# Optimization experiments

Hardware: AMD Instinct MI355X
Metric: run time of the kernel (lower is better)

## Reference

```python
import jax, jax.numpy as jnp
import numpy as np

G = 8          # n_games
D_IN = 512     # per-game input dim (equal for all games)
H1 = 1024
H2 = 1024
A = 128        # max_actions
B = 8192       # batch rows


def setup_inputs() -> dict:
    key = jax.random.key(0)
    ks = jax.random.split(key, 9)
    state = jax.random.normal(ks[0], (B, D_IN), dtype=jnp.float32)
    idx = jax.random.randint(ks[1], (B,), 0, G, dtype=jnp.int32)
    # per-game input linears: uniform(-1/sqrt(fan_in), 1/sqrt(fan_in))
    lim1 = 1.0 / np.sqrt(D_IN)
    W1 = jax.random.uniform(ks[2], (G, D_IN, H1), minval=-lim1, maxval=lim1, dtype=jnp.float32)
    b1 = jax.random.uniform(ks[3], (G, H1), minval=-lim1, maxval=lim1, dtype=jnp.float32)
    # shared linear
    lim2 = 1.0 / np.sqrt(H1)
    W2 = jax.random.uniform(ks[4], (H1, H2), minval=-lim2, maxval=lim2, dtype=jnp.float32)
    b2 = jax.random.uniform(ks[5], (H2,), minval=-lim2, maxval=lim2, dtype=jnp.float32)
    # per-game output heads: uniform(-0.003, 0.003)
    W3 = jax.random.uniform(ks[6], (G, H2, A), minval=-0.003, maxval=0.003, dtype=jnp.float32)
    b3 = jax.random.uniform(ks[7], (G, A), minval=-0.003, maxval=0.003, dtype=jnp.float32)
    return {"state": state, "idx": idx, "W1": W1, "b1": b1, "W2": W2, "b2": b2, "W3": W3, "b3": b3}


def reference(state, idx, W1, b1, W2, b2, W3, b3):
    # Torch code concatenates per-game groups in sorted-unique-idx order,
    # i.e. a stable permutation of rows by idx; reproduce exactly.
    perm = jnp.argsort(idx, stable=True)          # [B]
    s = state[perm]                               # [B, D_IN]
    g = idx[perm]                                 # [B] game of each permuted row
    # routed first layer: compute all games then gather per-row game
    h1_all = jnp.einsum('bd,gdh->bgh', s, W1) + b1            # [B, G, H1]
    h1 = jax.nn.relu(jnp.take_along_axis(h1_all, g[:, None, None], axis=1)[:, 0, :])  # [B, H1]
    h_f = jax.nn.relu(h1 @ W2 + b2)                            # [B, H2]
    a = jnp.tanh(jnp.einsum('bh,gha->bga', h_f, W3) + b3)      # [B, G, A]
    # NOTE: original gathers heads with the ORIGINAL (unpermuted) idx,
    # even though rows of `a` are in permuted order. Reproduce faithfully.
    out = jnp.take_along_axis(a, idx[:, None, None], axis=1)[:, 0, :]  # [B, A]
    return out
```

## Files before the change

### kernel.cpp

```cpp
#include <hip/hip_runtime.h>
#include <math.h>

#define G_GAMES 8
#define D_IN 512
#define H1 1024
#define H2 1024
#define A_DIM 128
#define B_ROWS 8192

typedef short bf16x8 __attribute__((ext_vector_type(8)));
typedef float f32x4 __attribute__((ext_vector_type(4)));

#define WS_OFF   0u
#define WS_PERM  256u
#define WS_SPERM 33280u
#define WS_W1T   (WS_SPERM + B_ROWS*D_IN*2u)
#define WS_W2T   (WS_W1T + G_GAMES*D_IN*H1*2u)
#define WS_W3T   (WS_W2T + (unsigned)H1*H2*2u)
#define WS_H1    (WS_W3T + G_GAMES*H2*A_DIM*2u)
#define WS_HF    WS_SPERM

__device__ __forceinline__ unsigned short f2bf(float x) {
  union { float f; unsigned int u; } v; v.f = x;
  unsigned int r = v.u + 0x7fffu + ((v.u >> 16) & 1u);
  return (unsigned short)(r >> 16);
}

__device__ __forceinline__ void async_load16(const void* gptr, void* ldsptr) {
  __builtin_amdgcn_global_load_lds(
      (const __attribute__((address_space(1))) unsigned int*)gptr,
      (__attribute__((address_space(3))) unsigned int*)ldsptr,
      16, 0, 0);
}

__device__ void sort_256(const int* __restrict__ idx, int* __restrict__ perm,
                         int* __restrict__ off) {
  __shared__ int wtot[4][9];
  __shared__ int wbase[4][9];
  __shared__ int offs[9];
  const int t = threadIdx.x, lane = t & 63, wave = t >> 6;
  int my[32];
#pragma unroll
  for (int i = 0; i < 8; ++i) {
    const int4 a = *(const int4*)(idx + t * 32 + i * 4);
    my[i*4+0] = a.x; my[i*4+1] = a.y; my[i*4+2] = a.z; my[i*4+3] = a.w;
  }
  int local[8] = {0,0,0,0,0,0,0,0};
#pragma unroll
  for (int i = 0; i < 32; ++i) local[my[i]]++;
  int incl[8];
#pragma unroll
  for (int g = 0; g < 8; ++g) {
    int v = local[g];
#pragma unroll
    for (int d = 1; d < 64; d <<= 1) {
      const int n = __shfl_up(v, d);
      if (lane >= d) v += n;
    }
    incl[g] = v;
  }
  if (lane == 63) {
#pragma unroll
    for (int g = 0; g < 8; ++g) wtot[wave][g] = incl[g];
  }
  __syncthreads();
  if (t < 8) {
    int s = 0;
#pragma unroll
    for (int w = 0; w < 4; ++w) { wbase[w][t] = s; s += wtot[w][t]; }
    wtot[0][t] = s;
  }
  __syncthreads();
  if (t == 0) {
    int s = 0;
#pragma unroll
    for (int g = 0; g < 8; ++g) { offs[g] = s; off[g] = s; s += wtot[0][g]; }
    offs[8] = s; off[8] = s;
  }
  __syncthreads();
  int start[8];
#pragma unroll
  for (int g = 0; g < 8; ++g)
    start[g] = offs[g] + wbase[wave][g] + (incl[g] - local[g]);
#pragma unroll
  for (int i = 0; i < 32; ++i) {
    const int g = my[i];
    perm[start[g]++] = t * 32 + i;
  }
}

__device__ void trans_tile(const float* __restrict__ in,
                           unsigned short* __restrict__ out,
                           int R, int C, int xt, int yt, int z) {
  in  += (size_t)z * R * C;
  out += (size_t)z * R * C;
  __shared__ float tile[64][65];
  const int c0 = xt * 64, r0 = yt * 64;
  const int tx = threadIdx.x & 63, ty = threadIdx.x >> 6;
#pragma unroll
  for (int rr = ty; rr < 64; rr += 4)
    tile[rr][tx] = in[(size_t)(r0 + rr) * C + c0 + tx];
  __syncthreads();
#pragma unroll
  for (int cc = ty; cc < 64; cc += 4)
    out[(size_t)(c0 + cc) * R + r0 + tx] = f2bf(tile[tx][cc]);
}

__global__ __launch_bounds__(256) void k_pre1(const float* __restrict__ W1,
                                              const float* __restrict__ W2,
                                              const float* __restrict__ W3,
                                              const int* __restrict__ idx,
                                              unsigned short* __restrict__ W1T,
                                              unsigned short* __restrict__ W2T,
                                              unsigned short* __restrict__ W3T,
                                              int* __restrict__ perm,
                                              int* __restrict__ off) {
  const int b = blockIdx.x;
  if (b < 1024) {
    const int z = b >> 7, r = b & 127;
    trans_tile(W1, W1T, D_IN, H1, r & 15, r >> 4, z);
  } else if (b < 1280) {
    const int r = b - 1024;
    trans_tile(W2, W2T, H1, H2, r & 15, r >> 4, 0);
  } else if (b < 1536) {
    const int r = (b - 1280) & 31, z = (b - 1280) >> 5;
    trans_tile(W3, W3T, H2, A_DIM, r & 1, r >> 1, z);
  } else {
    sort_256(idx, perm, off);
  }
}

__global__ __launch_bounds__(256) void k_gather(const float* __restrict__ state,
                                                const int* __restrict__ perm,
                                                unsigned short* __restrict__ sPerm) {
  const int p = blockIdx.x * 2 + (threadIdx.x >> 7);
  const int c = (threadIdx.x & 127) << 2;
  const int src = perm[p];
  const float4 v = *(const float4*)(state + (size_t)src * D_IN + c);
  ushort4 o;
  o.x = f2bf(v.x); o.y = f2bf(v.y); o.z = f2bf(v.z); o.w = f2bf(v.w);
  *(ushort4*)(sPerm + (size_t)p * D_IN + c) = o;
}

__device__ __forceinline__ void gemm_core128(const unsigned short* const* aP,
                                             const unsigned short* const* bP,
                                             char* A, char* Bc,
                                             int KTOT, int tid, f32x4 acc[4][4]) {
  const int lane = tid & 63, wave = tid >> 6;
  const int wm = wave & 1, wn = wave >> 1;
  const int mA = wm * 64 + (lane & 15);
  const int nB = wn * 64 + (lane & 15);
  const int quad = lane >> 4;
  const int sw = lane & 15;
  for (int k0 = 0; k0 < KTOT; k0 += 128) {
    __syncthreads();
#pragma unroll
    for (int c = 0; c < 8; ++c) {
      const int rbase = wave * 32 + c * 4;
      async_load16(aP[c] + k0, A + rbase * 256);
      async_load16(bP[c] + k0, Bc + rbase * 256);
    }
    __syncthreads();
#pragma unroll
    for (int ks = 0; ks < 4; ++ks) {
      const int u = (((ks * 4 + quad) ^ sw) << 4);
      bf16x8 aF[4], bF[4];
#pragma unroll
      for (int i = 0; i < 4; ++i) {
        aF[i] = *(const bf16x8*)(A + (mA + i * 16) * 256 + u);
        bF[i] = *(const bf16x8*)(Bc + (nB + i * 16) * 256 + u);
      }
#pragma unroll
      for (int i = 0; i < 4; ++i)
#pragma unroll
        for (int j = 0; j < 4; ++j)
          acc[i][j] = __builtin_amdgcn_mfma_f32_16x16x32_bf16(aF[i], bF[j], acc[i][j], 0, 0, 0);
    }
  }
}

__device__ __forceinline__ bool seg_map(const int* __restrict__ off, int T,
                                        int& g, int& seg1, int& row0) {
  int base = 0;
  for (int gg = 0; gg < 8; ++gg) {
    const int s = off[gg], e = off[gg + 1];
    const int nt = (e - s + 127) >> 7;
    if (T < base + nt) { g = gg; seg1 = e; row0 = s + (T - base) * 128; return true; }
    base += nt;
  }
  return false;
}

__device__ __forceinline__ bool seg_map32(const int* __restrict__ off, int T,
                                          int& g, int& seg1, int& row0) {
  int base = 0;
  for (int gg = 0; gg < 8; ++gg) {
    const int s = off[gg], e = off[gg + 1];
    const int nt = (e - s + 31) >> 5;
    if (T < base + nt) { g = gg; seg1 = e; row0 = s + (T - base) * 32; return true; }
    base += nt;
  }
  return false;
}

__global__ __launch_bounds__(256) void k_gemm1(const unsigned short* __restrict__ sPerm,
                                               const unsigned short* __restrict__ W1T,
                                               const float* __restrict__ b1,
                                               const int* __restrict__ off,
                                               unsigned short* __restrict__ h1out) {
  __shared__ unsigned short ldsA[128 * 128];
  __shared__ unsigned short ldsB[128 * 128];
  int g, seg1, row0;
  if (!seg_map(off, blockIdx.x, g, seg1, row0)) return;
  const int col0 = blockIdx.y * 128;
  const int tid = threadIdx.x, lane = tid & 63, wave = tid >> 6;
  const int quad = lane >> 4, sw = lane & 15;
  const unsigned short* aP[8];
  const unsigned short* bP[8];
#pragma unroll
  for (int c = 0; c < 8; ++c) {
    const int rl = wave * 32 + c * 4 + quad;
    const int srcoff = ((sw ^ (rl & 15)) << 3);
    int p = row0 + rl;
    if (p > seg1 - 1) p = seg1 - 1;
    aP[c] = sPerm + (size_t)p * D_IN + srcoff;
    bP[c] = W1T + (size_t)g * H1 * D_IN + (size_t)(col0 + rl) * D_IN + srcoff;
  }
  f32x4 acc[4][4] = {};
  gemm_core128(aP, bP, (char*)ldsA, (char*)ldsB, D_IN, tid, acc);
  const int wm = wave & 1, wn = wave >> 1;
  const float* bg = b1 + g * H1;
#pragma unroll
  for (int j = 0; j < 4; ++j) {
    const int n = col0 + wn * 64 + j * 16 + sw;
    const float bj = bg[n];
#pragma unroll
    for (int i = 0; i < 4; ++i) {
      const int rbase = row0 + wm * 64 + i * 16 + (quad << 2);
#pragma unroll
      for (int r = 0; r < 4; ++r) {
        const int p = rbase + r;
        if (p < seg1) {
          float v = acc[i][j][r] + bj;
          v = fmaxf(v, 0.0f);
          h1out[(size_t)p * H1 + n] = f2bf(v);
        }
      }
    }
  }
}

__global__ __launch_bounds__(256) void k_gemm2(const unsigned short* __restrict__ h1in,
                                               const unsigned short* __restrict__ W2T,
                                               const float* __restrict__ b2,
                                               unsigned short* __restrict__ hfout) {
  __shared__ unsigned short ldsA[128 * 128];
  __shared__ unsigned short ldsB[128 * 128];
  const int row0 = blockIdx.x * 128, col0 = blockIdx.y * 128;
  const int tid = threadIdx.x, lane = tid & 63, wave = tid >> 6;
  const int quad = lane >> 4, sw = lane & 15;
  const unsigned short* aP[8];
  const unsigned short* bP[8];
#pragma unroll
  for (int c = 0; c < 8; ++c) {
    const int rl = wave * 32 + c * 4 + quad;
    const int srcoff = ((sw ^ (rl & 15)) << 3);
    aP[c] = h1in + (size_t)(row0 + rl) * H1 + srcoff;
    bP[c] = W2T + (size_t)(col0 + rl) * H1 + srcoff;
  }
  f32x4 acc[4][4] = {};
  gemm_core128(aP, bP, (char*)ldsA, (char*)ldsB, H1, tid, acc);
  const int wm = wave & 1, wn = wave >> 1;
#pragma unroll
  for (int j = 0; j < 4; ++j) {
    const int n = col0 + wn * 64 + j * 16 + sw;
    const float bj = b2[n];
#pragma unroll
    for (int i = 0; i < 4; ++i) {
      const int rbase = row0 + wm * 64 + i * 16 + (quad << 2);
#pragma unroll
      for (int r = 0; r < 4; ++r) {
        float v = acc[i][j][r] + bj;
        v = fmaxf(v, 0.0f);
        hfout[(size_t)(rbase + r) * H2 + n] = f2bf(v);
      }
    }
  }
}

__global__ __launch_bounds__(256) void k_gemm3(const unsigned short* __restrict__ hf,
                                               const unsigned short* __restrict__ W3T,
                                               const float* __restrict__ b3,
                                               const int* __restrict__ off,
                                               const int* __restrict__ perm,
                                               float* __restrict__ outp) {
  __shared__ unsigned short ldsA[32 * 128];
  __shared__ unsigned short ldsB[128 * 128];
  int g, seg1, row0;
  if (!seg_map32(off, blockIdx.x, g, seg1, row0)) return;
  const int tid = threadIdx.x, lane = tid & 63, wave = tid >> 6;
  const int wm = wave & 1, wn = wave >> 1;
  const int quad = lane >> 4, sw = lane & 15;
  const unsigned short* aP[2];
  const unsigned short* bP[8];
#pragma unroll
  for (int c = 0; c < 2; ++c) {
    const int rl = wave * 8 + c * 4 + quad;
    const int srcoff = ((sw ^ (rl & 15)) << 3);
    int q = row0 + rl;
    if (q > seg1 - 1) q = seg1 - 1;
    aP[c] = hf + (size_t)perm[q] * H2 + srcoff;
  }
#pragma unroll
  for (int c = 0; c < 8; ++c) {
    const int rl = wave * 32 + c * 4 + quad;
    const int srcoff = ((sw ^ (rl & 15)) << 3);
    bP[c] = W3T + (size_t)g * A_DIM * H2 + (size_t)rl * H2 + srcoff;
  }
  char* A = (char*)ldsA;
  char* Bc = (char*)ldsB;
  const int mA = wm * 16 + sw;
  const int nB = wn * 64 + sw;
  f32x4 acc[4] = {};
  for (int k0 = 0; k0 < H2; k0 += 128) {
    __syncthreads();
#pragma unroll
    for (int c = 0; c < 2; ++c)
      async_load16(aP[c] + k0, A + (wave * 8 + c * 4) * 256);
#pragma unroll
    for (int c = 0; c < 8; ++c)
      async_load16(bP[c] + k0, Bc + (wave * 32 + c * 4) * 256);
    __syncthreads();
#pragma unroll
    for (int ks = 0; ks < 4; ++ks) {
      const int u = (((ks * 4 + quad) ^ sw) << 4);
      const bf16x8 aF = *(const bf16x8*)(A + mA * 256 + u);
      bf16x8 bF[4];
#pragma unroll
      for (int j = 0; j < 4; ++j)
        bF[j] = *(const bf16x8*)(Bc + (nB + j * 16) * 256 + u);
#pragma unroll
      for (int j = 0; j < 4; ++j)
        acc[j] = __builtin_amdgcn_mfma_f32_16x16x32_bf16(aF, bF[j], acc[j], 0, 0, 0);
    }
  }
  const float* bg = b3 + g * A_DIM;
#pragma unroll
  for (int j = 0; j < 4; ++j) {
    const int n = wn * 64 + j * 16 + sw;
    const float bj = bg[n];
    const int qbase = row0 + wm * 16 + (quad << 2);
#pragma unroll
    for (int r = 0; r < 4; ++r) {
      const int q2 = qbase + r;
      if (q2 < seg1)
        outp[(size_t)perm[q2] * A_DIM + n] = tanhf(acc[j][r] + bj);
    }
  }
}

extern "C" void kernel_launch(void* const* d_in, const int* in_sizes, int n_in,
                              void* d_out, int out_size, void* d_ws, size_t ws_size,
                              hipStream_t stream) {
  (void)in_sizes; (void)n_in; (void)out_size; (void)ws_size;
  const float* state = (const float*)d_in[0];
  const int*   idx   = (const int*)d_in[1];
  const float* W1    = (const float*)d_in[2];
  const float* b1    = (const float*)d_in[3];
  const float* W2    = (const float*)d_in[4];
  const float* b2    = (const float*)d_in[5];
  const float* W3    = (const float*)d_in[6];
  const float* b3    = (const float*)d_in[7];
  float* outp = (float*)d_out;
  char* ws = (char*)d_ws;
  int* off  = (int*)(ws + WS_OFF);
  int* perm = (int*)(ws + WS_PERM);
  unsigned short* sPerm = (unsigned short*)(ws + WS_SPERM);
  unsigned short* W1T   = (unsigned short*)(ws + WS_W1T);
  unsigned short* W2T   = (unsigned short*)(ws + WS_W2T);
  unsigned short* W3T   = (unsigned short*)(ws + WS_W3T);
  unsigned short* h1    = (unsigned short*)(ws + WS_H1);
  unsigned short* hf    = (unsigned short*)(ws + WS_HF);

  hipLaunchKernelGGL(k_pre1, dim3(1537), dim3(256), 0, stream,
                     W1, W2, W3, idx, W1T, W2T, W3T, perm, off);
  hipLaunchKernelGGL(k_gather, dim3(B_ROWS / 2), dim3(256), 0, stream, state, perm, sPerm);
  hipLaunchKernelGGL(k_gemm1, dim3(72, 8), dim3(256), 0, stream, sPerm, W1T, b1, off, h1);
  hipLaunchKernelGGL(k_gemm2, dim3(64, 8), dim3(256), 0, stream, h1, W2T, b2, hf);
  hipLaunchKernelGGL(k_gemm3, dim3(264), dim3(256), 0, stream, hf, W3T, b3, off, perm, outp);
}
```

Before: 172.3 us.

## Double-buffer GEMM K-loop with BK=64 and stage epilogues through LDS

Replaces the single-buffered BK=128 load-sync-compute loop in all three GEMMs with a double-buffered BK=64 pipeline, so async global-to-LDS loads of the next K slice are issued while MFMAs run on the current one, with one barrier per iteration. The swizzle changes to an 8-chunk XOR pattern to suit 128-byte LDS rows. The epilogues now stage bias+ReLU/tanh results in LDS and write 16-byte coalesced rows instead of scattered 2- or 4-byte stores. This costs extra LDS traffic and barriers in the epilogue, and smaller K slices mean more loop iterations.

```diff
diff --git a/kernel.cpp b/kernel.cpp
--- a/kernel.cpp
+++ b/kernel.cpp
@@ -142,33 +142,46 @@
   *(ushort4*)(sPerm + (size_t)p * D_IN + c) = o;
 }
 
-__device__ __forceinline__ void gemm_core128(const unsigned short* const* aP,
+template <int KTOT>
+__device__ __forceinline__ void gemm_db_core(const unsigned short* const* aP,
                                              const unsigned short* const* bP,
-                                             char* A, char* Bc,
-                                             int KTOT, int tid, f32x4 acc[4][4]) {
+                                             char* smem, int tid, f32x4 acc[4][4]) {
   const int lane = tid & 63, wave = tid >> 6;
   const int wm = wave & 1, wn = wave >> 1;
-  const int mA = wm * 64 + (lane & 15);
-  const int nB = wn * 64 + (lane & 15);
-  const int quad = lane >> 4;
-  const int sw = lane & 15;
-  for (int k0 = 0; k0 < KTOT; k0 += 128) {
+  const int sw = lane & 15, quad = lane >> 4;
+  const int mA = wm * 64 + sw;
+  const int nB = wn * 64 + sw;
+  char* A0 = smem;          char* A1 = smem + 16384;
+  char* B0 = smem + 32768;  char* B1 = smem + 49152;
+  const int NIT = KTOT >> 6;
+#pragma unroll
+  for (int c = 0; c < 4; ++c) {
+    async_load16(aP[c], A0 + (wave * 32 + c * 8) * 128);
+    async_load16(bP[c], B0 + (wave * 32 + c * 8) * 128);
+  }
+#pragma unroll 2
+  for (int k = 0; k < NIT; ++k) {
     __syncthreads();
-#pragma unroll
-    for (int c = 0; c < 8; ++c) {
-      const int rbase = wave * 32 + c * 4;
-      async_load16(aP[c] + k0, A + rbase * 256);
-      async_load16(bP[c] + k0, Bc + rbase * 256);
-    }
-    __syncthreads();
-#pragma unroll
-    for (int ks = 0; ks < 4; ++ks) {
-      const int u = (((ks * 4 + quad) ^ sw) << 4);
+    char* A = (k & 1) ? A1 : A0;
+    char* B = (k & 1) ? B1 : B0;
+    if (k + 1 < NIT) {
+      char* An = (k & 1) ? A0 : A1;
+      char* Bn = (k & 1) ? B0 : B1;
+      const int koff = (k + 1) << 6;
+#pragma unroll
+      for (int c = 0; c < 4; ++c) {
+        async_load16(aP[c] + koff, An + (wave * 32 + c * 8) * 128);
+        async_load16(bP[c] + koff, Bn + (wave * 32 + c * 8) * 128);
+      }
+    }
+#pragma unroll
+    for (int ks = 0; ks < 2; ++ks) {
+      const int u = ((((ks << 2) + quad) ^ (sw & 7)) << 4);
       bf16x8 aF[4], bF[4];
 #pragma unroll
       for (int i = 0; i < 4; ++i) {
-        aF[i] = *(const bf16x8*)(A + (mA + i * 16) * 256 + u);
-        bF[i] = *(const bf16x8*)(Bc + (nB + i * 16) * 256 + u);
+        aF[i] = *(const bf16x8*)(A + (mA + i * 16) * 128 + u);
+        bF[i] = *(const bf16x8*)(B + (nB + i * 16) * 128 + u);
       }
 #pragma unroll
       for (int i = 0; i < 4; ++i)
@@ -203,89 +216,95 @@
   return false;
 }
 
+__device__ __forceinline__ void epilogue_bf16(char* smem, const f32x4 acc[4][4],
+                                              const float* bj, int tid,
+                                              unsigned short* __restrict__ outp,
+                                              size_t ldOut, int row0, int col0,
+                                              int vrows) {
+  const int lane = tid & 63, wave = tid >> 6;
+  const int wm = wave & 1, wn = wave >> 1;
+  const int sw = lane & 15, quad = lane >> 4;
+  __syncthreads();
+#pragma unroll
+  for (int i = 0; i < 4; ++i)
+#pragma unroll
+    for (int j = 0; j < 4; ++j)
+#pragma unroll
+      for (int r = 0; r < 4; ++r) {
+        const int row = wm * 64 + i * 16 + quad * 4 + r;
+        const int col = wn * 64 + j * 16 + sw;
+        const float v = fmaxf(acc[i][j][r] + bj[j], 0.0f);
+        *(unsigned short*)(smem + row * 264 + col * 2) = f2bf(v);
+      }
+  __syncthreads();
+#pragma unroll
+  for (int q = 0; q < 8; ++q) {
+    const int idxq = q * 256 + tid;
+    const int row = idxq >> 4, ch = idxq & 15;
+    if (row < vrows) {
+      const uint2 lo = *(const uint2*)(smem + row * 264 + ch * 16);
+      const uint2 hi = *(const uint2*)(smem + row * 264 + ch * 16 + 8);
+      uint4 v; v.x = lo.x; v.y = lo.y; v.z = hi.x; v.w = hi.y;
+      *(uint4*)((char*)outp + ((size_t)(row0 + row) * ldOut + col0 + ch * 8) * 2) = v;
+    }
+  }
+}
+
 __global__ __launch_bounds__(256) void k_gemm1(const unsigned short* __restrict__ sPerm,
                                                const unsigned short* __restrict__ W1T,
                                                const float* __restrict__ b1,
                                                const int* __restrict__ off,
                                                unsigned short* __restrict__ h1out) {
-  __shared__ unsigned short ldsA[128 * 128];
-  __shared__ unsigned short ldsB[128 * 128];
+  __shared__ char smem[65536];
   int g, seg1, row0;
   if (!seg_map(off, blockIdx.x, g, seg1, row0)) return;
   const int col0 = blockIdx.y * 128;
   const int tid = threadIdx.x, lane = tid & 63, wave = tid >> 6;
-  const int quad = lane >> 4, sw = lane & 15;
-  const unsigned short* aP[8];
-  const unsigned short* bP[8];
-#pragma unroll
-  for (int c = 0; c < 8; ++c) {
-    const int rl = wave * 32 + c * 4 + quad;
-    const int srcoff = ((sw ^ (rl & 15)) << 3);
+  const int gcol = ((lane & 7) ^ (lane >> 3)) << 3;
+  const unsigned short* aP[4];
+  const unsigned short* bP[4];
+#pragma unroll
+  for (int c = 0; c < 4; ++c) {
+    const int rl = wave * 32 + c * 8 + (lane >> 3);
     int p = row0 + rl;
     if (p > seg1 - 1) p = seg1 - 1;
-    aP[c] = sPerm + (size_t)p * D_IN + srcoff;
-    bP[c] = W1T + (size_t)g * H1 * D_IN + (size_t)(col0 + rl) * D_IN + srcoff;
+    aP[c] = sPerm + (size_t)p * D_IN + gcol;
+    bP[c] = W1T + (size_t)g * H1 * D_IN + (size_t)(col0 + rl) * D_IN + gcol;
   }
   f32x4 acc[4][4] = {};
-  gemm_core128(aP, bP, (char*)ldsA, (char*)ldsB, D_IN, tid, acc);
-  const int wm = wave & 1, wn = wave >> 1;
+  gemm_db_core<D_IN>(aP, bP, smem, tid, acc);
+  const int wn = wave >> 1, sw = lane & 15;
   const float* bg = b1 + g * H1;
-#pragma unroll
-  for (int j = 0; j < 4; ++j) {
-    const int n = col0 + wn * 64 + j * 16 + sw;
-    const float bj = bg[n];
-#pragma unroll
-    for (int i = 0; i < 4; ++i) {
-      const int rbase = row0 + wm * 64 + i * 16 + (quad << 2);
-#pragma unroll
-      for (int r = 0; r < 4; ++r) {
-        const int p = rbase + r;
-        if (p < seg1) {
-          float v = acc[i][j][r] + bj;
-          v = fmaxf(v, 0.0f);
-          h1out[(size_t)p * H1 + n] = f2bf(v);
-        }
-      }
-    }
-  }
+  float bj[4];
+#pragma unroll
+  for (int j = 0; j < 4; ++j) bj[j] = bg[col0 + wn * 64 + j * 16 + sw];
+  const int vrows = min(128, seg1 - row0);
+  epilogue_bf16(smem, acc, bj, tid, h1out, H1, row0, col0, vrows);
 }
 
 __global__ __launch_bounds__(256) void k_gemm2(const unsigned short* __restrict__ h1in,
                                                const unsigned short* __restrict__ W2T,
                                                const float* __restrict__ b2,
                                                unsigned short* __restrict__ hfout) {
-  __shared__ unsigned short ldsA[128 * 128];
-  __shared__ unsigned short ldsB[128 * 128];
+  __shared__ char smem[65536];
   const int row0 = blockIdx.x * 128, col0 = blockIdx.y * 128;
   const int tid = threadIdx.x, lane = tid & 63, wave = tid >> 6;
-  const int quad = lane >> 4, sw = lane & 15;
-  const unsigned short* aP[8];
-  const unsigned short* bP[8];
-#pragma unroll
-  for (int c = 0; c < 8; ++c) {
-    const int rl = wave * 32 + c * 4 + quad;
-    const int srcoff = ((sw ^ (rl & 15)) << 3);
-    aP[c] = h1in + (size_t)(row0 + rl) * H1 + srcoff;
-    bP[c] = W2T + (size_t)(col0 + rl) * H1 + srcoff;
+  const int gcol = ((lane & 7) ^ (lane >> 3)) << 3;
+  const unsigned short* aP[4];
+  const unsigned short* bP[4];
+#pragma unroll
+  for (int c = 0; c < 4; ++c) {
+    const int rl = wave * 32 + c * 8 + (lane >> 3);
+    aP[c] = h1in + (size_t)(row0 + rl) * H1 + gcol;
+    bP[c] = W2T + (size_t)(col0 + rl) * H1 + gcol;
   }
   f32x4 acc[4][4] = {};
-  gemm_core128(aP, bP, (char*)ldsA, (char*)ldsB, H1, tid, acc);
-  const int wm = wave & 1, wn = wave >> 1;
-#pragma unroll
-  for (int j = 0; j < 4; ++j) {
-    const int n = col0 + wn * 64 + j * 16 + sw;
-    const float bj = b2[n];
-#pragma unroll
-    for (int i = 0; i < 4; ++i) {
-      const int rbase = row0 + wm * 64 + i * 16 + (quad << 2);
-#pragma unroll
-      for (int r = 0; r < 4; ++r) {
-        float v = acc[i][j][r] + bj;
-        v = fmaxf(v, 0.0f);
-        hfout[(size_t)(rbase + r) * H2 + n] = f2bf(v);
-      }
-    }
-  }
+  gemm_db_core<H1>(aP, bP, smem, tid, acc);
+  const int wn = wave >> 1, sw = lane & 15;
+  float bj[4];
+#pragma unroll
+  for (int j = 0; j < 4; ++j) bj[j] = b2[col0 + wn * 64 + j * 16 + sw];
+  epilogue_bf16(smem, acc, bj, tid, hfout, H2, row0, col0, 128);
 }
 
 __global__ __launch_bounds__(256) void k_gemm3(const unsigned short* __restrict__ hf,
@@ -294,67 +313,79 @@
                                                const int* __restrict__ off,
                                                const int* __restrict__ perm,
                                                float* __restrict__ outp) {
-  __shared__ unsigned short ldsA[32 * 128];
-  __shared__ unsigned short ldsB[128 * 128];
+  __shared__ char smem[40960];
   int g, seg1, row0;
   if (!seg_map32(off, blockIdx.x, g, seg1, row0)) return;
   const int tid = threadIdx.x, lane = tid & 63, wave = tid >> 6;
   const int wm = wave & 1, wn = wave >> 1;
-  const int quad = lane >> 4, sw = lane & 15;
-  const unsigned short* aP[2];
-  const unsigned short* bP[8];
-#pragma unroll
-  for (int c = 0; c < 2; ++c) {
-    const int rl = wave * 8 + c * 4 + quad;
-    const int srcoff = ((sw ^ (rl & 15)) << 3);
-    int q = row0 + rl;
-    if (q > seg1 - 1) q = seg1 - 1;
-    aP[c] = hf + (size_t)perm[q] * H2 + srcoff;
-  }
-#pragma unroll
-  for (int c = 0; c < 8; ++c) {
-    const int rl = wave * 32 + c * 4 + quad;
-    const int srcoff = ((sw ^ (rl & 15)) << 3);
-    bP[c] = W3T + (size_t)g * A_DIM * H2 + (size_t)rl * H2 + srcoff;
-  }
-  char* A = (char*)ldsA;
-  char* Bc = (char*)ldsB;
+  const int sw = lane & 15, quad = lane >> 4;
+  const int gcol = ((lane & 7) ^ (lane >> 3)) << 3;
+  int q0 = row0 + wave * 8 + (lane >> 3);
+  if (q0 > seg1 - 1) q0 = seg1 - 1;
+  const unsigned short* aP = hf + (size_t)perm[q0] * H2 + gcol;
+  const unsigned short* bP[4];
+#pragma unroll
+  for (int c = 0; c < 4; ++c) {
+    const int rl = wave * 32 + c * 8 + (lane >> 3);
+    bP[c] = W3T + (size_t)g * A_DIM * H2 + (size_t)rl * H2 + gcol;
+  }
+  char* A0 = smem;         char* A1 = smem + 4096;
+  char* B0 = smem + 8192;  char* B1 = smem + 24576;
   const int mA = wm * 16 + sw;
   const int nB = wn * 64 + sw;
   f32x4 acc[4] = {};
-  for (int k0 = 0; k0 < H2; k0 += 128) {
+  async_load16(aP, A0 + (wave * 8) * 128);
+#pragma unroll
+  for (int c = 0; c < 4; ++c)
+    async_load16(bP[c], B0 + (wave * 32 + c * 8) * 128);
+#pragma unroll 2
+  for (int k = 0; k < (H2 >> 6); ++k) {
     __syncthreads();
-#pragma unroll
-    for (int c = 0; c < 2; ++c)
-      async_load16(aP[c] + k0, A + (wave * 8 + c * 4) * 256);
-#pragma unroll
-    for (int c = 0; c < 8; ++c)
-      async_load16(bP[c] + k0, Bc + (wave * 32 + c * 4) * 256);
-    __syncthreads();
-#pragma unroll
-    for (int ks = 0; ks < 4; ++ks) {
-      const int u = (((ks * 4 + quad) ^ sw) << 4);
-      const bf16x8 aF = *(const bf16x8*)(A + mA * 256 + u);
+    char* A = (k & 1) ? A1 : A0;
+    char* B = (k & 1) ? B1 : B0;
+    if (k + 1 < (H2 >> 6)) {
+      char* An = (k & 1) ? A0 : A1;
+      char* Bn = (k & 1) ? B0 : B1;
+      const int koff = (k + 1) << 6;
+      async_load16(aP + koff, An + (wave * 8) * 128);
+#pragma unroll
+      for (int c = 0; c < 4; ++c)
+        async_load16(bP[c] + koff, Bn + (wave * 32 + c * 8) * 128);
+    }
+#pragma unroll
+    for (int ks = 0; ks < 2; ++ks) {
+      const int u = ((((ks << 2) + quad) ^ (sw & 7)) << 4);
+      const bf16x8 aF = *(const bf16x8*)(A + mA * 128 + u);
       bf16x8 bF[4];
 #pragma unroll
       for (int j = 0; j < 4; ++j)
-        bF[j] = *(const bf16x8*)(Bc + (nB + j * 16) * 256 + u);
+        bF[j] = *(const bf16x8*)(B + (nB + j * 16) * 128 + u);
 #pragma unroll
       for (int j = 0; j < 4; ++j)
         acc[j] = __builtin_amdgcn_mfma_f32_16x16x32_bf16(aF, bF[j], acc[j], 0, 0, 0);
     }
   }
   const float* bg = b3 + g * A_DIM;
-#pragma unroll
-  for (int j = 0; j < 4; ++j) {
-    const int n = wn * 64 + j * 16 + sw;
-    const float bj = bg[n];
-    const int qbase = row0 + wm * 16 + (quad << 2);
+  float bj[4];
+#pragma unroll
+  for (int j = 0; j < 4; ++j) bj[j] = bg[wn * 64 + j * 16 + sw];
+  __syncthreads();
+#pragma unroll
+  for (int j = 0; j < 4; ++j)
 #pragma unroll
     for (int r = 0; r < 4; ++r) {
-      const int q2 = qbase + r;
-      if (q2 < seg1)
-        outp[(size_t)perm[q2] * A_DIM + n] = tanhf(acc[j][r] + bj);
+      const int row = wm * 16 + quad * 4 + r;
+      const int col = wn * 64 + j * 16 + sw;
+      *(float*)(smem + row * 528 + col * 4) = tanhf(acc[j][r] + bj[j]);
+    }
+  __syncthreads();
+#pragma unroll
+  for (int qq = 0; qq < 4; ++qq) {
+    const int idxq = qq * 256 + tid;
+    const int row = idxq >> 5, ch = idxq & 31;
+    if (row0 + row < seg1) {
+      const uint4 v = *(const uint4*)(smem + row * 528 + ch * 16);
+      *(uint4*)((char*)outp + ((size_t)perm[row0 + row] * A_DIM + ch * 4) * 4) = v;
     }
   }
 }
```

Measured after the change: 155.6 us. 1.11x faster.
